# Kernel tuning notes

Measured on AMD Instinct MI355X. Metric: run time of the kernel, lower is better.

## Reference

```python
import jax, jax.numpy as jnp
import numpy as np

B_SZ, L, D_MODEL = 2, 1024, 1024
D_INNER, D_STATE, D_CONV = 2048, 16, 4
EPS = 1e-6


def setup_inputs() -> dict:
    key = jax.random.key(0)
    ks = jax.random.split(key, 8)
    def n(k, shape, scale=0.02):
        return jax.random.normal(k, shape, jnp.float32) * scale
    return {
        "x": jax.random.normal(ks[0], (B_SZ, L, D_MODEL), jnp.float32),
        "W_in": n(ks[1], (D_MODEL, 2 * D_INNER)),
        "b_in": jnp.zeros((2 * D_INNER,), jnp.float32),
        "conv_w": n(ks[2], (D_INNER, 1, D_CONV), 0.2),
        "conv_b": jnp.zeros((D_INNER,), jnp.float32),
        "W_xp": n(ks[3], (D_INNER, 2 * D_STATE)),
        "b_xp": jnp.zeros((2 * D_STATE,), jnp.float32),
        "W_dt": n(ks[4], (D_INNER, D_INNER)),
        "b_dt": jnp.full((D_INNER,), -1.0, jnp.float32),
        # torch code does log(randn) (NaN-prone); use log of positive uniform instead
        "A_log": jnp.log(jax.random.uniform(ks[5], (D_INNER, D_STATE), jnp.float32, 0.5, 1.5)),
        "D_skip": jnp.ones((D_INNER,), jnp.float32),
        "W_out": n(ks[6], (D_INNER, D_MODEL)),
        "b_out": jnp.zeros((D_MODEL,), jnp.float32),
        "alpha": jnp.ones((D_MODEL,), jnp.float32),
        "beta": jnp.zeros((D_MODEL,), jnp.float32),
    }


def _selective_scan(xc, delta, A, Bm, Cm, D_skip):
    # xc, delta: (B,L,di); A: (di,ds); Bm, Cm: (B,L,ds)
    dA = jnp.exp(delta[..., None] * A)                     # (B,L,di,ds)
    dBx = (delta * xc)[..., None] * Bm[:, :, None, :]      # (B,L,di,ds)
    h0 = jnp.zeros((xc.shape[0], xc.shape[2], A.shape[1]), xc.dtype)

    def step(h, inp):
        dA_t, dBx_t, C_t = inp
        h = dA_t * h + dBx_t                               # (B,di,ds)
        y_t = jnp.einsum('bds,bs->bd', h, C_t)
        return h, y_t

    _, ys = jax.lax.scan(
        step, h0,
        (dA.transpose(1, 0, 2, 3), dBx.transpose(1, 0, 2, 3), Cm.transpose(1, 0, 2)))
    y = ys.transpose(1, 0, 2)                              # (B,L,di)
    return y + D_skip * xc


def _layernorm(r, alpha, beta):
    # torch LayerNormalization: unbiased std, eps added to std
    mean = jnp.mean(r, axis=-1, keepdims=True)
    diff = r - mean
    var_unb = jnp.sum(diff * diff, axis=-1, keepdims=True) / (r.shape[-1] - 1)
    std = jnp.sqrt(var_unb)
    return alpha * diff / (std + EPS) + beta


def reference(x, W_in, b_in, conv_w, conv_b, W_xp, b_xp, W_dt, b_dt,
              A_log, D_skip, W_out, b_out, alpha, beta):
    residual = x
    xz = x @ W_in + b_in                                   # (B,L,2*di)
    x_in, z = jnp.split(xz, 2, axis=-1)

    # depthwise causal conv1d (torch pads d_conv-1 both sides, slices [:L])
    xt = x_in.transpose(0, 2, 1)                           # (B,di,L)
    xt = jax.lax.conv_general_dilated(
        xt, conv_w, window_strides=(1,), padding=[(D_CONV - 1, 0)],
        feature_group_count=D_INNER, dimension_numbers=('NCH', 'OIH', 'NCH'))
    xt = xt + conv_b[None, :, None]
    x_conv = jax.nn.silu(xt.transpose(0, 2, 1))            # (B,L,di)

    x_proj_out = x_conv @ W_xp + b_xp                      # (B,L,2*ds)
    Bm, Cm = jnp.split(x_proj_out, 2, axis=-1)
    delta = jax.nn.softplus(x_conv @ W_dt + b_dt)          # (B,L,di)
    A = -jnp.exp(A_log)

    y = _selective_scan(x_conv, delta, A, Bm, Cm, D_skip)
    y = y * jax.nn.silu(z)
    out = y @ W_out + b_out                                # (B,L,D)
    return _layernorm(residual + out, alpha, beta)
```

## Files before the change

kernel.cpp:

```cpp
#include <hip/hip_runtime.h>
#include <math.h>

#define B_SZ    2
#define L_SEQ   1024
#define DMODEL  1024
#define DINNER  2048
#define DSTATE  16
#define EPSV    1e-6f

#define CCH 64
#define CS  (L_SEQ / CCH)
#define DT  16
#define SSTR2 (CCH * DT + 2)

typedef short  bf16x8  __attribute__((ext_vector_type(8)));
typedef float  floatx4 __attribute__((ext_vector_type(4)));
typedef unsigned short ushort8v __attribute__((ext_vector_type(8)));

extern "C" __device__ float __ocml_native_exp2_f32(float);
extern "C" __device__ float __ocml_native_log2_f32(float);

__device__ __forceinline__ float nexp2(float x) { return __ocml_native_exp2_f32(x); }

__device__ __forceinline__ float softplus_f(float v) {
    if (v > 20.f) return v;
    return 0.69314718f * __ocml_native_log2_f32(1.f + nexp2(v * 1.44269504f));
}
__device__ __forceinline__ float silu_f(float z) {
    return z / (1.f + nexp2(z * -1.44269504f));
}

__device__ __forceinline__ unsigned short f2bf(float f) {
    unsigned int u = __float_as_uint(f);
    unsigned int r = (u + 0x7FFFu + ((u >> 16) & 1u)) >> 16;
    return (unsigned short)r;
}
__device__ __forceinline__ float bf2f(unsigned short u) {
    return __uint_as_float(((unsigned int)u) << 16);
}

__global__ __launch_bounds__(256) void prep_kernel(
    const float* __restrict__ x, unsigned short* __restrict__ x_bf,
    const float* __restrict__ W_in, unsigned short* __restrict__ W_in_t,
    const float* __restrict__ W_dt, unsigned short* __restrict__ W_dt_t,
    const float* __restrict__ W_out, unsigned short* __restrict__ W_out_t)
{
    const int bid = blockIdx.x;
    if (bid >= 10240) {
        const int i = (bid - 10240) * 256 + threadIdx.x;
        float4 v = ((const float4*)x)[i];
        ushort4 o = { f2bf(v.x), f2bf(v.y), f2bf(v.z), f2bf(v.w) };
        ((ushort4*)x_bf)[i] = o;
        return;
    }
    __shared__ float tile[32][33];
    const float* W; unsigned short* Wt; int K, N, t;
    if (bid < 4096)      { W = W_in;  Wt = W_in_t;  K = 1024; N = 4096; t = bid; }
    else if (bid < 8192) { W = W_dt;  Wt = W_dt_t;  K = 2048; N = 2048; t = bid - 4096; }
    else                 { W = W_out; Wt = W_out_t; K = 2048; N = 1024; t = bid - 8192; }
    const int nx = N >> 5;
    const int n0 = (t % nx) * 32;
    const int k0 = (t / nx) * 32;
    const int c = threadIdx.x & 31;
    const int r = threadIdx.x >> 5;
#pragma unroll
    for (int i = 0; i < 4; ++i)
        tile[r + 8 * i][c] = W[(size_t)(k0 + r + 8 * i) * N + n0 + c];
    __syncthreads();
#pragma unroll
    for (int i = 0; i < 4; ++i)
        Wt[(size_t)(n0 + r + 8 * i) * K + k0 + c] = f2bf(tile[c][r + 8 * i]);
}

template <int TM, int TN, int MODE, int MINW>
__global__ __launch_bounds__(256, MINW) void gemm_bf16(
    const unsigned short* __restrict__ A, const unsigned short* __restrict__ Bt,
    const float* __restrict__ bias, const float* __restrict__ resid,
    float* __restrict__ C, int M, int N, int K)
{
    constexpr int MI = TM / 32;
    constexpr int NJ = TN / 32;
    constexpr int NLOAD = (TM + TN) / 32;

    __shared__ unsigned short As[TM * 64];
    __shared__ unsigned short Bs[TN * 64];

    const int tid  = threadIdx.x;
    const int wave = tid >> 6;
    const int lane = tid & 63;
    const int m0 = blockIdx.y * TM;
    const int n0 = blockIdx.x * TN;
    const int wm = (wave >> 1) * (TM / 2);
    const int wn = (wave & 1) * (TN / 2);
    const int fr = lane & 15;
    const int kg = lane >> 4;

    int offs[NLOAD];
    unsigned short* lp[NLOAD];
#pragma unroll
    for (int i = 0; i < NLOAD; ++i) {
        const int slot = i * 256 + tid;
        const int row  = slot >> 3;
        const int ch   = slot & 7;
        const int pos  = ch ^ (row & 7);
        if (i < TM / 32) {
            offs[i] = (m0 + row) * K + ch * 8;
            lp[i]   = &As[row * 64 + pos * 8];
        } else {
            const int rb = row - TM;
            offs[i] = (n0 + rb) * K + ch * 8;
            lp[i]   = &Bs[rb * 64 + pos * 8];
        }
    }

    floatx4 acc[MI][NJ] = {};
    bf16x8 pre[NLOAD];

#pragma unroll
    for (int i = 0; i < NLOAD; ++i)
        pre[i] = *(const bf16x8*)((i < TM / 32 ? A : Bt) + offs[i]);
#pragma unroll
    for (int i = 0; i < NLOAD; ++i)
        *(bf16x8*)lp[i] = pre[i];
    __syncthreads();

    for (int kt = 0; kt < K; kt += 64) {
        const bool more = (kt + 64) < K;
        if (more) {
#pragma unroll
            for (int i = 0; i < NLOAD; ++i)
                pre[i] = *(const bf16x8*)((i < TM / 32 ? A : Bt) + offs[i] + kt + 64);
        }

#pragma unroll
        for (int ks = 0; ks < 2; ++ks) {
            const int cq = (ks << 2) | kg;
            bf16x8 af[MI], bfv[NJ];
#pragma unroll
            for (int i = 0; i < MI; ++i) {
                const int row = wm + i * 16 + fr;
                af[i] = *(const bf16x8*)&As[row * 64 + ((cq ^ (row & 7)) << 3)];
            }
#pragma unroll
            for (int j = 0; j < NJ; ++j) {
                const int row = wn + j * 16 + fr;
                bfv[j] = *(const bf16x8*)&Bs[row * 64 + ((cq ^ (row & 7)) << 3)];
            }
#pragma unroll
            for (int i = 0; i < MI; ++i)
#pragma unroll
                for (int j = 0; j < NJ; ++j)
                    acc[i][j] = __builtin_amdgcn_mfma_f32_16x16x32_bf16(
                        af[i], bfv[j], acc[i][j], 0, 0, 0);
        }
        __syncthreads();
        if (more) {
#pragma unroll
            for (int i = 0; i < NLOAD; ++i)
                *(bf16x8*)lp[i] = pre[i];
        }
        __syncthreads();
    }

    const int rq = (lane >> 4) * 4;
    if (MODE == 4) {
        unsigned short* Ct = (unsigned short*)C;
#pragma unroll
        for (int i = 0; i < MI; ++i) {
#pragma unroll
            for (int j = 0; j < NJ; ++j) {
                const int col = n0 + wn + j * 16 + fr;
                const float bv = bias[col];
                const int row0 = m0 + wm + i * 16 + rq;
                ushort4 o;
#pragma unroll
                for (int r = 0; r < 4; ++r)
                    (&o.x)[r] = f2bf(softplus_f(acc[i][j][r] + bv));
                *(ushort4*)&Ct[(size_t)col * M + row0] = o;
            }
        }
    } else {
#pragma unroll
        for (int i = 0; i < MI; ++i) {
#pragma unroll
            for (int j = 0; j < NJ; ++j) {
                const int col = n0 + wn + j * 16 + fr;
                const float bv = bias[col];
#pragma unroll
                for (int r = 0; r < 4; ++r) {
                    const int row = m0 + wm + i * 16 + rq + r;
                    float v = acc[i][j][r] + bv;
                    if (MODE == 1) {
                        v = softplus_f(v);
                    } else if (MODE == 2) {
                        v += resid[(size_t)row * N + col];
                    }
                    C[(size_t)row * N + col] = v;
                }
            }
        }
    }
}

#define CROWS 4
__global__ __launch_bounds__(256) void conv_xproj(
    const float* __restrict__ xz, const float* __restrict__ conv_w,
    const float* __restrict__ conv_b, const float* __restrict__ W_xp,
    const float* __restrict__ b_xp,
    unsigned short* __restrict__ x_conv_bf, float* __restrict__ BC)
{
    __shared__ float sxc[CROWS][DINNER];
    __shared__ float red[8][CROWS][32];

    const int tid = threadIdx.x;
    const int r0 = blockIdx.x * CROWS;
    const int c8 = tid * 8;

    float wt[8][4];
#pragma unroll
    for (int ci = 0; ci < 8; ++ci) {
        float4 w4 = *(const float4*)&conv_w[(c8 + ci) * 4];
        wt[ci][0] = w4.x; wt[ci][1] = w4.y; wt[ci][2] = w4.z; wt[ci][3] = w4.w;
    }
    float cb[8];
    *(float4*)&cb[0] = *(const float4*)&conv_b[c8];
    *(float4*)&cb[4] = *(const float4*)&conv_b[c8 + 4];

#pragma unroll
    for (int rr = 0; rr < CROWS; ++rr) {
        const int row = r0 + rr;
        const int l = row & (L_SEQ - 1);
        float acc[8];
#pragma unroll
        for (int ci = 0; ci < 8; ++ci) acc[ci] = cb[ci];
#pragma unroll
        for (int h = 0; h < 4; ++h) {
            const int lsrc = l - 3 + h;
            if (lsrc >= 0) {
                float4 a = *(const float4*)&xz[(size_t)(row - 3 + h) * (2 * DINNER) + c8];
                float4 b = *(const float4*)&xz[(size_t)(row - 3 + h) * (2 * DINNER) + c8 + 4];
                acc[0] += a.x * wt[0][h]; acc[1] += a.y * wt[1][h];
                acc[2] += a.z * wt[2][h]; acc[3] += a.w * wt[3][h];
                acc[4] += b.x * wt[4][h]; acc[5] += b.y * wt[5][h];
                acc[6] += b.z * wt[6][h]; acc[7] += b.w * wt[7][h];
            }
        }
        float o[8];
        ushort8v ob;
#pragma unroll
        for (int ci = 0; ci < 8; ++ci) {
            o[ci] = silu_f(acc[ci]);
            sxc[rr][c8 + ci] = o[ci];
            ob[ci] = (short)f2bf(o[ci]);
        }
        *(ushort8v*)&x_conv_bf[(size_t)row * DINNER + c8] = ob;
    }
    __syncthreads();

    const int n = tid & 31;
    const int g = tid >> 5;
    float p[CROWS] = {};
    const int k0 = g * 256;
#pragma unroll 4
    for (int k = k0; k < k0 + 256; ++k) {
        const float wv = W_xp[k * 32 + n];
        p[0] += sxc[0][k] * wv;
        p[1] += sxc[1][k] * wv;
        p[2] += sxc[2][k] * wv;
        p[3] += sxc[3][k] * wv;
    }
#pragma unroll
    for (int rr = 0; rr < CROWS; ++rr) red[g][rr][n] = p[rr];
    __syncthreads();
    if (tid < CROWS * 32) {
        const int rr = tid >> 5;
        const int n2 = tid & 31;
        float s = b_xp[n2];
#pragma unroll
        for (int gg = 0; gg < 8; ++gg) s += red[gg][rr][n2];
        BC[(size_t)(r0 + rr) * 32 + n2] = s;
    }
}

__global__ __launch_bounds__(1024, 4) void scan_kernel(
    const unsigned short* __restrict__ deltaT,
    const unsigned short* __restrict__ xc_bf,
    const float* __restrict__ BC, const float* __restrict__ A_log,
    const float* __restrict__ D_skip, const float* __restrict__ xz,
    unsigned short* __restrict__ y_bf)
{
    __shared__ unsigned short sA[DSTATE * SSTR2];
    __shared__ unsigned short sH[DSTATE * SSTR2];

    const int tid = threadIdx.x;
    const int dl  = tid & (DT - 1);
    const int c   = tid >> 4;
    const int b   = blockIdx.x >> 7;
    const int d0  = (blockIdx.x & 127) * DT;
    const int d   = d0 + dl;

    float Al[DSTATE];
#pragma unroll
    for (int s = 0; s < DSTATE; ++s)
        Al[s] = -__expf(A_log[d * DSTATE + s]) * 1.44269504f;
    const float Dsk = D_skip[d];

    const int l0 = c * CS;
    const int row0 = b * L_SEQ + l0;

    const unsigned short* dpt = deltaT + (size_t)d * (B_SZ * L_SEQ) + row0;
    bf16x8 dv0 = *(const bf16x8*)dpt;
    bf16x8 dv1 = *(const bf16x8*)(dpt + 8);
    float dts[CS];
    float dsum = 0.f;
#pragma unroll
    for (int k = 0; k < 8; ++k) {
        dts[k]     = bf2f((unsigned short)dv0[k]);
        dts[8 + k] = bf2f((unsigned short)dv1[k]);
    }
#pragma unroll
    for (int k = 0; k < CS; ++k) dsum += dts[k];

    float h[DSTATE];
#pragma unroll
    for (int s = 0; s < DSTATE; ++s) h[s] = 0.f;

    const unsigned short* xcp = xc_bf + (size_t)row0 * DINNER + d;
    const float* bcp = BC + (size_t)row0 * 32;

#pragma unroll 4
    for (int j = 0; j < CS; ++j) {
        const float dt = dts[j];
        const float xc = bf2f(xcp[j * DINNER]);
        float Bv[DSTATE];
        *(float4*)&Bv[0]  = *(const float4*)(bcp + j * 32 + 0);
        *(float4*)&Bv[4]  = *(const float4*)(bcp + j * 32 + 4);
        *(float4*)&Bv[8]  = *(const float4*)(bcp + j * 32 + 8);
        *(float4*)&Bv[12] = *(const float4*)(bcp + j * 32 + 12);
        const float dlx = dt * xc;
#pragma unroll
        for (int s = 0; s < DSTATE; ++s) {
            const float e = nexp2(dt * Al[s]);
            h[s] = e * h[s] + dlx * Bv[s];
        }
    }
#pragma unroll
    for (int s = 0; s < DSTATE; ++s) {
        sH[s * SSTR2 + c * DT + dl] = f2bf(h[s]);
        sA[s * SSTR2 + c * DT + dl] = f2bf(nexp2(Al[s] * dsum));
    }
    __syncthreads();

    if (tid < DSTATE * DT) {
        const int dl2 = tid & (DT - 1);
        const int s2  = tid >> 4;
        float hh = 0.f;
#pragma unroll
        for (int c2 = 0; c2 < CCH; ++c2) {
            const int idx = s2 * SSTR2 + c2 * DT + dl2;
            const float a  = bf2f(sA[idx]);
            const float he = bf2f(sH[idx]);
            sH[idx] = f2bf(hh);
            hh = a * hh + he;
        }
    }
    __syncthreads();

#pragma unroll
    for (int s = 0; s < DSTATE; ++s) h[s] = bf2f(sH[s * SSTR2 + c * DT + dl]);

    const float* zp = xz + (size_t)row0 * (2 * DINNER) + DINNER + d;
    unsigned short* yp = y_bf + (size_t)row0 * DINNER + d;
#pragma unroll 4
    for (int j = 0; j < CS; ++j) {
        const float dt = dts[j];
        const float xc = bf2f(xcp[j * DINNER]);
        const float z  = zp[j * (2 * DINNER)];
        float Bv[DSTATE], Cv[DSTATE];
        *(float4*)&Bv[0]  = *(const float4*)(bcp + j * 32 + 0);
        *(float4*)&Bv[4]  = *(const float4*)(bcp + j * 32 + 4);
        *(float4*)&Bv[8]  = *(const float4*)(bcp + j * 32 + 8);
        *(float4*)&Bv[12] = *(const float4*)(bcp + j * 32 + 12);
        *(float4*)&Cv[0]  = *(const float4*)(bcp + j * 32 + 16);
        *(float4*)&Cv[4]  = *(const float4*)(bcp + j * 32 + 20);
        *(float4*)&Cv[8]  = *(const float4*)(bcp + j * 32 + 24);
        *(float4*)&Cv[12] = *(const float4*)(bcp + j * 32 + 28);
        const float dlx = dt * xc;
        float y = Dsk * xc;
#pragma unroll
        for (int s = 0; s < DSTATE; ++s) {
            const float e = nexp2(dt * Al[s]);
            h[s] = e * h[s] + dlx * Bv[s];
            y += h[s] * Cv[s];
        }
        yp[j * DINNER] = f2bf(y * silu_f(z));
    }
}

__global__ __launch_bounds__(256) void layernorm_kernel(
    const float* __restrict__ t, const float* __restrict__ alpha,
    const float* __restrict__ beta, float* __restrict__ out)
{
    __shared__ float sred[4];
    __shared__ float sred2[4];
    const int row = blockIdx.x;
    const int tid = threadIdx.x;
    const float* r = t + (size_t)row * DMODEL;

    float4 v = *(const float4*)&r[tid * 4];
    float lsum = v.x + v.y + v.z + v.w;
#pragma unroll
    for (int m = 1; m < 64; m <<= 1) lsum += __shfl_xor(lsum, m);
    if ((tid & 63) == 0) sred[tid >> 6] = lsum;
    __syncthreads();
    const float mean = (sred[0] + sred[1] + sred[2] + sred[3]) * (1.f / DMODEL);

    const float dx = v.x - mean, dy = v.y - mean, dz = v.z - mean, dw = v.w - mean;
    float ls2 = dx * dx + dy * dy + dz * dz + dw * dw;
#pragma unroll
    for (int m = 1; m < 64; m <<= 1) ls2 += __shfl_xor(ls2, m);
    if ((tid & 63) == 0) sred2[tid >> 6] = ls2;
    __syncthreads();
    const float var = (sred2[0] + sred2[1] + sred2[2] + sred2[3]) * (1.f / (DMODEL - 1));
    const float inv = 1.f / (sqrtf(var) + EPSV);

    float4 a4 = *(const float4*)&alpha[tid * 4];
    float4 b4 = *(const float4*)&beta[tid * 4];
    float4 o;
    o.x = a4.x * dx * inv + b4.x;
    o.y = a4.y * dy * inv + b4.y;
    o.z = a4.z * dz * inv + b4.z;
    o.w = a4.w * dw * inv + b4.w;
    *(float4*)&out[(size_t)row * DMODEL + tid * 4] = o;
}

extern "C" void kernel_launch(void* const* d_in, const int* in_sizes, int n_in,
                              void* d_out, int out_size, void* d_ws, size_t ws_size,
                              hipStream_t stream)
{
    const float* x      = (const float*)d_in[0];
    const float* W_in   = (const float*)d_in[1];
    const float* b_in   = (const float*)d_in[2];
    const float* conv_w = (const float*)d_in[3];
    const float* conv_b = (const float*)d_in[4];
    const float* W_xp   = (const float*)d_in[5];
    const float* b_xp   = (const float*)d_in[6];
    const float* W_dt   = (const float*)d_in[7];
    const float* b_dt   = (const float*)d_in[8];
    const float* A_log  = (const float*)d_in[9];
    const float* D_skip = (const float*)d_in[10];
    const float* W_out  = (const float*)d_in[11];
    const float* b_out  = (const float*)d_in[12];
    const float* alpha  = (const float*)d_in[13];
    const float* beta   = (const float*)d_in[14];
    float* out = (float*)d_out;

    const size_t M = (size_t)B_SZ * L_SEQ;
    char* ws = (char*)d_ws;
    float* xz      = (float*)(ws + 0);
    unsigned short* deltaT = (unsigned short*)(ws + (48u << 20));
    float* BC      = (float*)(ws + (64u << 20));
    unsigned short* x_bf       = (unsigned short*)(ws + (64u << 20) + (512u << 10));
    unsigned short* W_in_t     = (unsigned short*)(ws + (69u << 20));
    unsigned short* W_dt_t     = (unsigned short*)(ws + (77u << 20));
    unsigned short* W_out_t    = (unsigned short*)(ws + (85u << 20));
    unsigned short* x_conv_bf  = (unsigned short*)(ws + (89u << 20));
    unsigned short* ygate_bf   = (unsigned short*)(ws + (77u << 20));
    float* tpre = xz;

    const dim3 blk(256);

    prep_kernel<<<dim3(12288), blk, 0, stream>>>(
        x, x_bf, W_in, W_in_t, W_dt, W_dt_t, W_out, W_out_t);

    gemm_bf16<128, 128, 0, 2><<<dim3(4096 / 128, 2048 / 128), blk, 0, stream>>>(
        x_bf, W_in_t, b_in, nullptr, xz, 2048, 4096, 1024);

    conv_xproj<<<dim3((unsigned)(M / CROWS)), blk, 0, stream>>>(
        xz, conv_w, conv_b, W_xp, b_xp, x_conv_bf, BC);

    gemm_bf16<128, 64, 4, 3><<<dim3(2048 / 64, 2048 / 128), blk, 0, stream>>>(
        x_conv_bf, W_dt_t, b_dt, nullptr, (float*)deltaT, 2048, 2048, 2048);

    scan_kernel<<<dim3(B_SZ * (DINNER / DT)), dim3(1024), 0, stream>>>(
        deltaT, x_conv_bf, BC, A_log, D_skip, xz, ygate_bf);

    gemm_bf16<64, 64, 2, 3><<<dim3(1024 / 64, 2048 / 64), blk, 0, stream>>>(
        ygate_bf, W_out_t, b_out, x, tpre, 2048, 1024, 2048);

    layernorm_kernel<<<dim3((unsigned)M), blk, 0, stream>>>(tpre, alpha, beta, out);
}
```

Measured before the change: 270.1 us.

## Fuse silu(z) gating into in-proj GEMM epilogue and stage x_conv in LDS

```diff
diff --git a/kernel.cpp b/kernel.cpp
--- a/kernel.cpp
+++ b/kernel.cpp
@@ -76,7 +76,8 @@
 __global__ __launch_bounds__(256, MINW) void gemm_bf16(
     const unsigned short* __restrict__ A, const unsigned short* __restrict__ Bt,
     const float* __restrict__ bias, const float* __restrict__ resid,
-    float* __restrict__ C, int M, int N, int K)
+    float* __restrict__ C, unsigned short* __restrict__ zout,
+    int M, int N, int K)
 {
     constexpr int MI = TM / 32;
     constexpr int NJ = TN / 32;
@@ -179,6 +180,37 @@
                 *(ushort4*)&Ct[(size_t)col * M + row0] = o;
             }
         }
+    } else if (MODE == 5) {
+        if (n0 < DINNER) {
+#pragma unroll
+            for (int i = 0; i < MI; ++i) {
+#pragma unroll
+                for (int j = 0; j < NJ; ++j) {
+                    const int col = n0 + wn + j * 16 + fr;
+                    const float bv = bias[col];
+#pragma unroll
+                    for (int r = 0; r < 4; ++r) {
+                        const int row = m0 + wm + i * 16 + rq + r;
+                        C[(size_t)row * DINNER + col] = acc[i][j][r] + bv;
+                    }
+                }
+            }
+        } else {
+#pragma unroll
+            for (int i = 0; i < MI; ++i) {
+#pragma unroll
+                for (int j = 0; j < NJ; ++j) {
+                    const int col = n0 + wn + j * 16 + fr;
+                    const float bv = bias[col];
+                    const int row0 = m0 + wm + i * 16 + rq;
+                    ushort4 o;
+#pragma unroll
+                    for (int r = 0; r < 4; ++r)
+                        (&o.x)[r] = f2bf(silu_f(acc[i][j][r] + bv));
+                    *(ushort4*)&zout[(size_t)(col - DINNER) * M + row0] = o;
+                }
+            }
+        }
     } else {
 #pragma unroll
         for (int i = 0; i < MI; ++i) {
@@ -204,7 +236,7 @@
 
 #define CROWS 4
 __global__ __launch_bounds__(256) void conv_xproj(
-    const float* __restrict__ xz, const float* __restrict__ conv_w,
+    const float* __restrict__ x_in, const float* __restrict__ conv_w,
     const float* __restrict__ conv_b, const float* __restrict__ W_xp,
     const float* __restrict__ b_xp,
     unsigned short* __restrict__ x_conv_bf, float* __restrict__ BC)
@@ -237,8 +269,8 @@
         for (int h = 0; h < 4; ++h) {
             const int lsrc = l - 3 + h;
             if (lsrc >= 0) {
-                float4 a = *(const float4*)&xz[(size_t)(row - 3 + h) * (2 * DINNER) + c8];
-                float4 b = *(const float4*)&xz[(size_t)(row - 3 + h) * (2 * DINNER) + c8 + 4];
+                float4 a = *(const float4*)&x_in[(size_t)(row - 3 + h) * DINNER + c8];
+                float4 b = *(const float4*)&x_in[(size_t)(row - 3 + h) * DINNER + c8 + 4];
                 acc[0] += a.x * wt[0][h]; acc[1] += a.y * wt[1][h];
                 acc[2] += a.z * wt[2][h]; acc[3] += a.w * wt[3][h];
                 acc[4] += b.x * wt[4][h]; acc[5] += b.y * wt[5][h];
@@ -286,11 +318,12 @@
     const unsigned short* __restrict__ deltaT,
     const unsigned short* __restrict__ xc_bf,
     const float* __restrict__ BC, const float* __restrict__ A_log,
-    const float* __restrict__ D_skip, const float* __restrict__ xz,
+    const float* __restrict__ D_skip, const unsigned short* __restrict__ zt,
     unsigned short* __restrict__ y_bf)
 {
     __shared__ unsigned short sA[DSTATE * SSTR2];
     __shared__ unsigned short sH[DSTATE * SSTR2];
+    __shared__ unsigned short sxc[(L_SEQ + L_SEQ / 16) * 16];
 
     const int tid = threadIdx.x;
     const int dl  = tid & (DT - 1);
@@ -299,6 +332,16 @@
     const int d0  = (blockIdx.x & 127) * DT;
     const int d   = d0 + dl;
 
+#pragma unroll
+    for (int i = 0; i < 2; ++i) {
+        const int slot = i * 1024 + tid;
+        const int t    = slot >> 1;
+        const int half = slot & 1;
+        ushort8v v = *(const ushort8v*)
+            &xc_bf[(size_t)(b * L_SEQ + t) * DINNER + d0 + half * 8];
+        *(ushort8v*)&sxc[(t + (t >> 4)) * 16 + half * 8] = v;
+    }
+
     float Al[DSTATE];
 #pragma unroll
     for (int s = 0; s < DSTATE; ++s)
@@ -311,6 +354,10 @@
     const unsigned short* dpt = deltaT + (size_t)d * (B_SZ * L_SEQ) + row0;
     bf16x8 dv0 = *(const bf16x8*)dpt;
     bf16x8 dv1 = *(const bf16x8*)(dpt + 8);
+    const unsigned short* gpt = zt + (size_t)d * (B_SZ * L_SEQ) + row0;
+    bf16x8 gv0 = *(const bf16x8*)gpt;
+    bf16x8 gv1 = *(const bf16x8*)(gpt + 8);
+
     float dts[CS];
     float dsum = 0.f;
 #pragma unroll
@@ -325,13 +372,14 @@
 #pragma unroll
     for (int s = 0; s < DSTATE; ++s) h[s] = 0.f;
 
-    const unsigned short* xcp = xc_bf + (size_t)row0 * DINNER + d;
     const float* bcp = BC + (size_t)row0 * 32;
 
-#pragma unroll 4
+    __syncthreads();
+
+#pragma unroll
     for (int j = 0; j < CS; ++j) {
         const float dt = dts[j];
-        const float xc = bf2f(xcp[j * DINNER]);
+        const float xc = bf2f(sxc[(c * 17 + j) * 16 + dl]);
         float Bv[DSTATE];
         *(float4*)&Bv[0]  = *(const float4*)(bcp + j * 32 + 0);
         *(float4*)&Bv[4]  = *(const float4*)(bcp + j * 32 + 4);
@@ -355,7 +403,7 @@
         const int dl2 = tid & (DT - 1);
         const int s2  = tid >> 4;
         float hh = 0.f;
-#pragma unroll
+#pragma unroll 4
         for (int c2 = 0; c2 < CCH; ++c2) {
             const int idx = s2 * SSTR2 + c2 * DT + dl2;
             const float a  = bf2f(sA[idx]);
@@ -369,13 +417,12 @@
 #pragma unroll
     for (int s = 0; s < DSTATE; ++s) h[s] = bf2f(sH[s * SSTR2 + c * DT + dl]);
 
-    const float* zp = xz + (size_t)row0 * (2 * DINNER) + DINNER + d;
     unsigned short* yp = y_bf + (size_t)row0 * DINNER + d;
-#pragma unroll 4
+#pragma unroll
     for (int j = 0; j < CS; ++j) {
         const float dt = dts[j];
-        const float xc = bf2f(xcp[j * DINNER]);
-        const float z  = zp[j * (2 * DINNER)];
+        const float xc = bf2f(sxc[(c * 17 + j) * 16 + dl]);
+        const float g  = bf2f((unsigned short)(j < 8 ? gv0[j] : gv1[j - 8]));
         float Bv[DSTATE], Cv[DSTATE];
         *(float4*)&Bv[0]  = *(const float4*)(bcp + j * 32 + 0);
         *(float4*)&Bv[4]  = *(const float4*)(bcp + j * 32 + 4);
@@ -393,7 +440,7 @@
             h[s] = e * h[s] + dlx * Bv[s];
             y += h[s] * Cv[s];
         }
-        yp[j * DINNER] = f2bf(y * silu_f(z));
+        yp[j * DINNER] = f2bf(y * g);
     }
 }
 
@@ -457,7 +504,8 @@
 
     const size_t M = (size_t)B_SZ * L_SEQ;
     char* ws = (char*)d_ws;
-    float* xz      = (float*)(ws + 0);
+    float* x_in    = (float*)(ws + 0);
+    unsigned short* zt = (unsigned short*)(ws + (16u << 20));
     unsigned short* deltaT = (unsigned short*)(ws + (48u << 20));
     float* BC      = (float*)(ws + (64u << 20));
     unsigned short* x_bf       = (unsigned short*)(ws + (64u << 20) + (512u << 10));
@@ -466,27 +514,27 @@
     unsigned short* W_out_t    = (unsigned short*)(ws + (85u << 20));
     unsigned short* x_conv_bf  = (unsigned short*)(ws + (89u << 20));
     unsigned short* ygate_bf   = (unsigned short*)(ws + (77u << 20));
-    float* tpre = xz;
+    float* tpre = x_in;
 
     const dim3 blk(256);
 
     prep_kernel<<<dim3(12288), blk, 0, stream>>>(
         x, x_bf, W_in, W_in_t, W_dt, W_dt_t, W_out, W_out_t);
 
-    gemm_bf16<128, 128, 0, 2><<<dim3(4096 / 128, 2048 / 128), blk, 0, stream>>>(
-        x_bf, W_in_t, b_in, nullptr, xz, 2048, 4096, 1024);
+    gemm_bf16<128, 128, 5, 2><<<dim3(4096 / 128, 2048 / 128), blk, 0, stream>>>(
+        x_bf, W_in_t, b_in, nullptr, x_in, zt, 2048, 4096, 1024);
 
     conv_xproj<<<dim3((unsigned)(M / CROWS)), blk, 0, stream>>>(
-        xz, conv_w, conv_b, W_xp, b_xp, x_conv_bf, BC);
+        x_in, conv_w, conv_b, W_xp, b_xp, x_conv_bf, BC);
 
     gemm_bf16<128, 64, 4, 3><<<dim3(2048 / 64, 2048 / 128), blk, 0, stream>>>(
-        x_conv_bf, W_dt_t, b_dt, nullptr, (float*)deltaT, 2048, 2048, 2048);
+        x_conv_bf, W_dt_t, b_dt, nullptr, (float*)deltaT, nullptr, 2048, 2048, 2048);
 
     scan_kernel<<<dim3(B_SZ * (DINNER / DT)), dim3(1024), 0, stream>>>(
-        deltaT, x_conv_bf, BC, A_log, D_skip, xz, ygate_bf);
+        deltaT, x_conv_bf, BC, A_log, D_skip, zt, ygate_bf);
 
     gemm_bf16<64, 64, 2, 3><<<dim3(1024 / 64, 2048 / 64), blk, 0, stream>>>(
-        ygate_bf, W_out_t, b_out, x, tpre, 2048, 1024, 2048);
+        ygate_bf, W_out_t, b_out, x, tpre, nullptr, 2048, 1024, 2048);
 
     layernorm_kernel<<<dim3((unsigned)M), blk, 0, stream>>>(tpre, alpha, beta, out);
 }
```

Result: slower. 550.9 us (+103.9%).
